# Performance work log

Hardware: AMD Instinct MI355X
Metric: run time of the kernel (lower is better)

## Reference

```python
import jax, jax.numpy as jnp
import numpy as np

GAMMA = 0.7
WALK_LEN = 3
TAU = 1.0
N_FILTERS = 8


def _row_norm(A):
    return A / jnp.clip(jnp.sum(A, axis=-1, keepdims=True), 1e-12, None)


def _motif_channel(A, idx, Wadj, gates):
    # A: [n,n]; idx: [I,k] int node indices; Wadj: [F,k,k]; gates: [L]
    n = A.shape[0]
    I, k = idx.shape
    F = Wadj.shape[0]
    # learnable filter adjacency: softplus, symmetrize, zero diagonal, row-normalize
    S = jax.nn.softplus(Wadj)
    S = 0.5 * (S + jnp.swapaxes(S, -1, -2)) * (1.0 - jnp.eye(k, dtype=A.dtype))
    Sf = _row_norm(S)                                  # [F,k,k]
    # per-instance induced subgraph transition matrices
    As = A[idx[:, :, None], idx[:, None, :]]           # [I,k,k]
    Tm = _row_norm(As)                                 # [I,k,k]
    # batched Kronecker product: Km[i,f,a*k+b,c*k+d] = Tm[i,a,c]*Sf[f,b,d]
    Km = (Tm[:, None, :, None, :, None] * Sf[None, :, None, :, None, :]).reshape(I, F, k * k, k * k)
    gp = jax.nn.softplus(gates)                        # [L] length gates
    M = Km
    acc = (GAMMA * gp[0]) * jnp.trace(M, axis1=-2, axis2=-1)   # [I,F]
    for p in range(2, WALK_LEN + 1):
        M = M @ Km
        acc = acc + (GAMMA ** p * gp[p - 1]) * jnp.trace(M, axis1=-2, axis2=-1)
    sims = acc                                         # [I,F] RWK similarities
    alphas = jax.nn.softmax(sims / max(1e-06, TAU), axis=-1)
    contrib = (alphas * sims) / float(k)               # [I,F]
    upd = jnp.broadcast_to(contrib[:, None, :], (I, k, F)).reshape(I * k, F)
    return jnp.zeros((n, F), A.dtype).at[idx.reshape(-1)].add(upd)


def _layer(A, tri_idx, cyc_idx, H, Wt, Wc, g, lng, lnb, w1, b1, w2, b2):
    Phi = jnp.concatenate([_motif_channel(A, tri_idx, Wt, g),
                           _motif_channel(A, cyc_idx, Wc, g),
                           H], axis=1)                 # [n, in_ch]
    mu = jnp.mean(Phi, axis=-1, keepdims=True)
    var = jnp.var(Phi, axis=-1, keepdims=True)
    X = (Phi - mu) / jnp.sqrt(var + 1e-5) * lng + lnb  # LayerNorm
    return jax.nn.gelu(X @ w1 + b1, approximate=False) @ w2 + b2  # dropout = identity (eval)


def _templates():
    tri = np.zeros((3, 3), np.float32)
    for u, v in [(0, 1), (1, 2), (0, 2)]:
        tri[u, v] = tri[v, u] = 1.0
    cyc = np.zeros((4, 4), np.float32)
    for u, v in [(0, 1), (1, 2), (2, 3), (3, 0)]:
        cyc[u, v] = cyc[v, u] = 1.0
    return tri, cyc


def setup_inputs() -> dict:
    key = jax.random.key(0)
    ks = jax.random.split(key, 16)
    n, D, HID = 4096, 128, 128
    A = (jax.random.uniform(ks[0], (n, n)) < 0.01).astype(jnp.float32)
    A = 0.5 * (A + A.T)
    A = A * (1.0 - jnp.eye(n, dtype=jnp.float32))
    tri_idx = jax.random.randint(ks[1], (30000, 3), 0, n, dtype=jnp.int32)
    cyc_idx = jax.random.randint(ks[2], (15000, 4), 0, n, dtype=jnp.int32)
    tri_t, cyc_t = _templates()
    def w_adj(k, tmpl):
        return jnp.asarray(tmpl)[None] + 0.05 * jax.random.normal(k, (N_FILTERS,) + tmpl.shape, dtype=jnp.float32)
    in0, in1 = 17, 145
    inp = {"A_full": A, "tri_idx": tri_idx, "cyc_idx": cyc_idx,
           "W_tri_0": w_adj(ks[3], tri_t), "W_cyc_0": w_adj(ks[4], cyc_t),
           "gates_0": jnp.zeros((WALK_LEN,), jnp.float32),
           "lng_0": jnp.ones((in0,), jnp.float32), "lnb_0": jnp.zeros((in0,), jnp.float32),
           "w1_0": 0.05 * jax.random.normal(ks[5], (in0, HID), jnp.float32), "b1_0": jnp.zeros((HID,), jnp.float32),
           "w2_0": 0.05 * jax.random.normal(ks[6], (HID, D), jnp.float32), "b2_0": jnp.zeros((D,), jnp.float32),
           "W_tri_1": w_adj(ks[7], tri_t), "W_cyc_1": w_adj(ks[8], cyc_t),
           "gates_1": jnp.zeros((WALK_LEN,), jnp.float32),
           "lng_1": jnp.ones((in1,), jnp.float32), "lnb_1": jnp.zeros((in1,), jnp.float32),
           "w1_1": 0.05 * jax.random.normal(ks[9], (in1, HID), jnp.float32), "b1_1": jnp.zeros((HID,), jnp.float32),
           "w2_1": 0.05 * jax.random.normal(ks[10], (HID, D), jnp.float32), "b2_1": jnp.zeros((D,), jnp.float32)}
    return inp


def reference(A_full, tri_idx, cyc_idx,
              W_tri_0, W_cyc_0, gates_0, lng_0, lnb_0, w1_0, b1_0, w2_0, b2_0,
              W_tri_1, W_cyc_1, gates_1, lng_1, lnb_1, w1_1, b1_1, w2_1, b2_1):
    # base channel (use_base=True): node degree from dense adjacency
    H = jnp.sum(A_full, axis=-1, keepdims=True)        # [n,1]
    Z = _layer(A_full, tri_idx, cyc_idx, H, W_tri_0, W_cyc_0, gates_0, lng_0, lnb_0, w1_0, b1_0, w2_0, b2_0)
    H = jnp.concatenate([Z, H], axis=1)                # residual_cat: [n,129]
    Z = _layer(A_full, tri_idx, cyc_idx, H, W_tri_1, W_cyc_1, gates_1, lng_1, lnb_1, w1_1, b1_1, w2_1, b2_1)
    H = jnp.concatenate([Z, H], axis=1)                # [n,257]
    return H
```

## Files before the change

### kernel.cpp

```cpp
#include <hip/hip_runtime.h>
#include <math.h>
#include <stdint.h>

#define GAMMA 0.7f
#define CAP 96

typedef __attribute__((ext_vector_type(8))) short short8v;
typedef __attribute__((ext_vector_type(4))) float f32x4;

__device__ __forceinline__ float sp_dev(float x) {
    return fmaxf(x, 0.0f) + log1pf(expf(-fabsf(x)));
}
__device__ __forceinline__ float gelu_exact(float x) {
    return 0.5f * x * (1.0f + erff(x * 0.70710678118654752f));
}
__device__ __forceinline__ uint16_t f2bf(float x) {
    union { float f; uint32_t u; } c; c.f = x;
    uint32_t u = c.u + 0x7FFFu + ((c.u >> 16) & 1u);
    return (uint16_t)(u >> 16);
}

__global__ void prep_kernel(const float* __restrict__ Wt0, const float* __restrict__ Wc0,
                            const float* __restrict__ g0,
                            const float* __restrict__ Wt1, const float* __restrict__ Wc1,
                            const float* __restrict__ g1,
                            const float* __restrict__ w1_0, const float* __restrict__ w2_0,
                            const float* __restrict__ w1_1, const float* __restrict__ w2_1,
                            float* __restrict__ dcoef,
                            uint16_t* __restrict__ Wb10, uint16_t* __restrict__ Wb20,
                            uint16_t* __restrict__ Wb11, uint16_t* __restrict__ Wb21,
                            int* __restrict__ cursor, int ncur) {
    int tid = threadIdx.x;
    int gtid = blockIdx.x * blockDim.x + tid;
    int stride = gridDim.x * blockDim.x;

    for (int i = gtid; i < ncur; i += stride) cursor[i] = 0;

    if (blockIdx.x == 0 && tid < 32) {
        int L = tid >> 4, m = (tid >> 3) & 1, f = tid & 7;
        int k = m ? 4 : 3;
        const float* W = L ? (m ? Wc1 : Wt1) : (m ? Wc0 : Wt0);
        const float* g = L ? g1 : g0;
        float S[4][4], Y[4][4];
        for (int a = 0; a < k; a++)
            for (int b = 0; b < k; b++)
                S[a][b] = sp_dev(W[(f * k + a) * k + b]);
        for (int a = 0; a < k; a++)
            for (int b = 0; b < k; b++)
                Y[a][b] = (a == b) ? 0.0f : 0.5f * (S[a][b] + S[b][a]);
        for (int a = 0; a < k; a++) {
            float rs = 0.0f;
            for (int b = 0; b < k; b++) rs += Y[a][b];
            rs = fmaxf(rs, 1e-12f);
            for (int b = 0; b < k; b++) Y[a][b] /= rs;
        }
        float t1 = 0, t2 = 0, t3 = 0;
        for (int a = 0; a < k; a++) t1 += Y[a][a];
        for (int a = 0; a < k; a++)
            for (int b = 0; b < k; b++) t2 += Y[a][b] * Y[b][a];
        for (int a = 0; a < k; a++)
            for (int b = 0; b < k; b++)
                for (int c = 0; c < k; c++) t3 += Y[a][b] * Y[b][c] * Y[c][a];
        float* d = dcoef + ((L * 2 + m) * 8 + f) * 3;
        d[0] = GAMMA * sp_dev(g[0]) * t1;
        d[1] = GAMMA * GAMMA * sp_dev(g[1]) * t2;
        d[2] = GAMMA * GAMMA * GAMMA * sp_dev(g[2]) * t3;
    }
    for (int idx = gtid; idx < 57344; idx += stride) {
        if (idx < 4096) {
            int c = idx >> 5, k = idx & 31;
            Wb10[idx] = (k < 17) ? f2bf(w1_0[k * 128 + c]) : 0;
        } else if (idx < 20480) {
            int e = idx - 4096; int c = e >> 7, k = e & 127;
            Wb20[e] = f2bf(w2_0[k * 128 + c]);
        } else if (idx < 40960) {
            int e = idx - 20480; int c = e / 160, k = e % 160;
            Wb11[e] = (k < 145) ? f2bf(w1_1[k * 128 + c]) : 0;
        } else {
            int e = idx - 40960; int c = e >> 7, k = e & 127;
            Wb21[e] = f2bf(w2_1[k * 128 + c]);
        }
    }
}

template <int K>
__device__ __forceinline__ void contrib_group(
    const float* __restrict__ A, int n,
    const int* __restrict__ idx, int I, int i, int g, int lane,
    const float (*dc)[8][3], float* __restrict__ cont,
    int* __restrict__ cursor, int* __restrict__ slotbuf) {
    int base = lane & ~3;
    int mynode = (g < K) ? idx[i * K + g] : 0;
    int nb0 = __shfl(mynode, base + 0);
    int nb1 = __shfl(mynode, base + 1);
    int nb2 = __shfl(mynode, base + 2);
    int nb3 = (K == 4) ? __shfl(mynode, base + 3) : 0;

    float r0, r1, r2, r3;
    if (K == 3) {
        if (g < 3) {
            const float* Ar = A + (size_t)mynode * n;
            r0 = Ar[nb0]; r1 = Ar[nb1]; r2 = Ar[nb2]; r3 = 0.0f;
        } else {
            r0 = 0.0f; r1 = 0.0f; r2 = 0.0f; r3 = 1.0f;
        }
    } else {
        const float* Ar = A + (size_t)mynode * n;
        r0 = Ar[nb0]; r1 = Ar[nb1]; r2 = Ar[nb2]; r3 = Ar[nb3];
    }
    float rs = fmaxf(r0 + r1 + r2 + r3, 1e-12f);
    float inv = 1.0f / rs;
    r0 *= inv; r1 *= inv; r2 *= inv; r3 *= inv;

    float M[4][4];
#pragma unroll
    for (int b = 0; b < 4; b++) {
        M[b][0] = __shfl(r0, base + b);
        M[b][1] = __shfl(r1, base + b);
        M[b][2] = __shfl(r2, base + b);
        M[b][3] = __shfl(r3, base + b);
    }

    float t1 = M[0][0] + M[1][1] + M[2][2] + M[3][3];
    float t2 = 0.0f, t3 = 0.0f;
#pragma unroll
    for (int a = 0; a < 4; a++)
#pragma unroll
        for (int b = 0; b < 4; b++) {
            float ab = M[a][b];
            t2 += ab * M[b][a];
#pragma unroll
            for (int c = 0; c < 4; c++) t3 += ab * M[b][c] * M[c][a];
        }
    if (K == 3) { t1 -= 1.0f; t2 -= 1.0f; t3 -= 1.0f; }

#pragma unroll
    for (int L = 0; L < 2; L++) {
        float sims[8], mx = -1e30f;
#pragma unroll
        for (int f = 0; f < 8; f++) {
            sims[f] = dc[L][f][0] * t1 + dc[L][f][1] * t2 + dc[L][f][2] * t3;
            mx = fmaxf(mx, sims[f]);
        }
        float es[8], se = 0.0f;
#pragma unroll
        for (int f = 0; f < 8; f++) { es[f] = expf(sims[f] - mx); se += es[f]; }
        float sinv = 1.0f / se;
        float cn[8];
#pragma unroll
        for (int f = 0; f < 8; f++) cn[f] = es[f] * sinv * sims[f] * (1.0f / (float)K);
        float p0 = (g == 0) ? cn[0] : (g == 1) ? cn[2] : (g == 2) ? cn[4] : cn[6];
        float p1 = (g == 0) ? cn[1] : (g == 1) ? cn[3] : (g == 2) ? cn[5] : cn[7];
        float2 st = make_float2(p0, p1);
        *(float2*)(cont + ((size_t)L * I + i) * 8 + 2 * g) = st;
    }

    if (g < K) {
        int pos = atomicAdd(&cursor[mynode], 1);
        if (pos < CAP) slotbuf[(size_t)mynode * CAP + pos] = i;
    }
}

__global__ __launch_bounds__(256) void fused_kernel(
    const float* __restrict__ A, int n,
    const int* __restrict__ tri, int Itri,
    const int* __restrict__ cyc, int Icyc,
    int Btri, int Bcyc,
    const float* __restrict__ dcoef,
    float* __restrict__ tri_c, float* __restrict__ cyc_c,
    int* __restrict__ cursor, int* __restrict__ slotbuf,
    float* __restrict__ H0, float* __restrict__ out) {
    __shared__ float dc[2][8][3];
    __shared__ float red[4];
    int bid = blockIdx.x;
    int tid = threadIdx.x;

    if (bid < Btri + Bcyc) {
        bool isTri = bid < Btri;
        const float* dl0 = dcoef + (isTri ? 0 : 24);
        const float* dl1 = dcoef + (isTri ? 48 : 72);
        if (tid < 24) dc[0][tid / 3][tid % 3] = dl0[tid];
        else if (tid < 48) { int t = tid - 24; dc[1][t / 3][t % 3] = dl1[t]; }
        __syncthreads();

        int lane = tid & 63;
        int g = tid & 3;
        if (isTri) {
            int i = bid * 64 + (tid >> 2);
            if (i < Itri)
                contrib_group<3>(A, n, tri, Itri, i, g, lane, dc, tri_c, cursor, slotbuf);
        } else {
            int i = (bid - Btri) * 64 + (tid >> 2);
            if (i < Icyc)
                contrib_group<4>(A, n, cyc, Icyc, i, g, lane, dc, cyc_c,
                                 cursor + n, slotbuf + (size_t)n * CAP);
        }
    } else {
        int row = bid - (Btri + Bcyc);
        const float4* Arow = (const float4*)(A + (size_t)row * n);
        int n4 = n >> 2;
        float s = 0.0f;
        for (int i = tid; i < n4; i += 256) {
            float4 v = Arow[i];
            s += v.x + v.y + v.z + v.w;
        }
        for (int off = 32; off > 0; off >>= 1) s += __shfl_down(s, off);
        if ((tid & 63) == 0) red[tid >> 6] = s;
        __syncthreads();
        if (tid == 0) {
            float t = red[0] + red[1] + red[2] + red[3];
            H0[row] = t;
            out[(size_t)row * 257 + 256] = t;
        }
    }
}

__global__ __launch_bounds__(512) void mega_kernel(
    const float* __restrict__ tri_c, int Itri,
    const float* __restrict__ cyc_c, int Icyc,
    const int* __restrict__ cursor, const int* __restrict__ slotbuf,
    const float* __restrict__ H0,
    const float* __restrict__ lng0, const float* __restrict__ lnb0,
    const uint16_t* __restrict__ Wb10, const float* __restrict__ b1_0,
    const uint16_t* __restrict__ Wb20, const float* __restrict__ b2_0,
    const float* __restrict__ lng1, const float* __restrict__ lnb1,
    const uint16_t* __restrict__ Wb11, const float* __restrict__ b1_1,
    const uint16_t* __restrict__ Wb21, const float* __restrict__ b2_1,
    float* __restrict__ out, int n) {
    __shared__ uint16_t Xs[16][168];
    __shared__ uint16_t Hs[16][136];
    __shared__ float    Zs[16][129];
    __shared__ float    phi0[16][17];
    __shared__ float    f1[16][16];
    __shared__ float    h0s[16];

    int tid = threadIdx.x;
    int v0 = blockIdx.x * 16;
    int wave = tid >> 6;
    int lane = tid & 63;
    int lr = lane & 15, lg = lane >> 4;

    {
        int r = tid >> 5;
        int combo = tid & 31;
        int m = combo >> 4, L = (combo >> 3) & 1, f = combo & 7;
        int v = v0 + r;
        int cnt = cursor[m * n + v];
        cnt = cnt < CAP ? cnt : CAP;
        const int* bucket = slotbuf + ((size_t)(m * n + v)) * CAP;
        const float* c = m ? cyc_c : tri_c;
        int I = m ? Icyc : Itri;
        float sum = 0.0f;
        for (int j = 0; j < cnt; j++) {
            int i = bucket[j];
            sum += c[((size_t)L * I + i) * 8 + f];
        }
        if (L == 0) phi0[r][m * 8 + f] = sum;
        else        f1[r][m * 8 + f] = sum;
        if (combo == 0) { float h = H0[v]; phi0[r][16] = h; h0s[r] = h; }
    }
    __syncthreads();

    {
        int r = tid >> 5;
        int j = tid & 31;
        float x = (j < 17) ? phi0[r][j] : 0.0f;
        float s1 = x, s2 = x * x;
        for (int o = 16; o > 0; o >>= 1) { s1 += __shfl_xor(s1, o); s2 += __shfl_xor(s2, o); }
        float mu = s1 / 17.0f;
        float rstd = rsqrtf(s2 / 17.0f - mu * mu + 1e-5f);
        Xs[r][j] = (j < 17) ? f2bf((x - mu) * rstd * lng0[j] + lnb0[j]) : (uint16_t)0;
    }
    __syncthreads();

    {
        int col = wave * 16 + lr;
        f32x4 acc = {0.f, 0.f, 0.f, 0.f};
        short8v a = *(const short8v*)&Xs[lr][lg * 8];
        short8v b = *(const short8v*)(Wb10 + (size_t)col * 32 + lg * 8);
        acc = __builtin_amdgcn_mfma_f32_16x16x32_bf16(a, b, acc, 0, 0, 0);
        float bias = b1_0[col];
#pragma unroll
        for (int i = 0; i < 4; i++)
            Hs[lg * 4 + i][col] = f2bf(gelu_exact(acc[i] + bias));
    }
    __syncthreads();

    {
        int col = wave * 16 + lr;
        f32x4 acc = {0.f, 0.f, 0.f, 0.f};
#pragma unroll
        for (int ks = 0; ks < 4; ks++) {
            short8v a = *(const short8v*)&Hs[lr][ks * 32 + lg * 8];
            short8v b = *(const short8v*)(Wb20 + (size_t)col * 128 + ks * 32 + lg * 8);
            acc = __builtin_amdgcn_mfma_f32_16x16x32_bf16(a, b, acc, 0, 0, 0);
        }
        float bias = b2_0[col];
#pragma unroll
        for (int i = 0; i < 4; i++) {
            int row = lg * 4 + i;
            float val = acc[i] + bias;
            out[(size_t)(v0 + row) * 257 + 128 + col] = val;
            Zs[row][col] = val;
        }
    }
    __syncthreads();

    {
        int rr = tid >> 5;
        int t = tid & 31;
        float ph[5];
        float s1 = 0.0f, s2 = 0.0f;
#pragma unroll
        for (int s = 0; s < 5; s++) {
            int j = t + 32 * s;
            float x = 0.0f;
            if (j < 16) x = f1[rr][j];
            else if (j < 144) x = Zs[rr][j - 16];
            else if (j == 144) x = h0s[rr];
            ph[s] = x;
            if (j < 145) { s1 += x; s2 += x * x; }
        }
        for (int o = 16; o > 0; o >>= 1) { s1 += __shfl_xor(s1, o); s2 += __shfl_xor(s2, o); }
        float mu = s1 / 145.0f;
        float rstd = rsqrtf(s2 / 145.0f - mu * mu + 1e-5f);
#pragma unroll
        for (int s = 0; s < 5; s++) {
            int j = t + 32 * s;
            Xs[rr][j] = (j < 145) ? f2bf((ph[s] - mu) * rstd * lng1[j] + lnb1[j]) : (uint16_t)0;
        }
    }
    __syncthreads();

    {
        int col = wave * 16 + lr;
        f32x4 acc = {0.f, 0.f, 0.f, 0.f};
#pragma unroll
        for (int ks = 0; ks < 5; ks++) {
            short8v a = *(const short8v*)&Xs[lr][ks * 32 + lg * 8];
            short8v b = *(const short8v*)(Wb11 + (size_t)col * 160 + ks * 32 + lg * 8);
            acc = __builtin_amdgcn_mfma_f32_16x16x32_bf16(a, b, acc, 0, 0, 0);
        }
        float bias = b1_1[col];
#pragma unroll
        for (int i = 0; i < 4; i++)
            Hs[lg * 4 + i][col] = f2bf(gelu_exact(acc[i] + bias));
    }
    __syncthreads();

    {
        int col = wave * 16 + lr;
        f32x4 acc = {0.f, 0.f, 0.f, 0.f};
#pragma unroll
        for (int ks = 0; ks < 4; ks++) {
            short8v a = *(const short8v*)&Hs[lr][ks * 32 + lg * 8];
            short8v b = *(const short8v*)(Wb21 + (size_t)col * 128 + ks * 32 + lg * 8);
            acc = __builtin_amdgcn_mfma_f32_16x16x32_bf16(a, b, acc, 0, 0, 0);
        }
        float bias = b2_1[col];
#pragma unroll
        for (int i = 0; i < 4; i++) {
            int row = lg * 4 + i;
            out[(size_t)(v0 + row) * 257 + col] = acc[i] + bias;
        }
    }
}

extern "C" void kernel_launch(void* const* d_in, const int* in_sizes, int n_in,
                              void* d_out, int out_size, void* d_ws, size_t ws_size,
                              hipStream_t stream) {
    const float* A    = (const float*)d_in[0];
    const int*   tri  = (const int*)d_in[1];
    const int*   cyc  = (const int*)d_in[2];
    const float* Wt0  = (const float*)d_in[3];
    const float* Wc0  = (const float*)d_in[4];
    const float* g0   = (const float*)d_in[5];
    const float* lng0 = (const float*)d_in[6];
    const float* lnb0 = (const float*)d_in[7];
    const float* w1_0 = (const float*)d_in[8];
    const float* b1_0 = (const float*)d_in[9];
    const float* w2_0 = (const float*)d_in[10];
    const float* b2_0 = (const float*)d_in[11];
    const float* Wt1  = (const float*)d_in[12];
    const float* Wc1  = (const float*)d_in[13];
    const float* g1   = (const float*)d_in[14];
    const float* lng1 = (const float*)d_in[15];
    const float* lnb1 = (const float*)d_in[16];
    const float* w1_1 = (const float*)d_in[17];
    const float* b1_1 = (const float*)d_in[18];
    const float* w2_1 = (const float*)d_in[19];
    const float* b2_1 = (const float*)d_in[20];

    int n    = out_size / 257;
    int Itri = in_sizes[1] / 3;
    int Icyc = in_sizes[2] / 4;

    float* ws    = (float*)d_ws;
    float* dcoef = ws;
    float* H0    = ws + 128;
    float* tri_c = H0 + n;
    float* cyc_c = tri_c + (size_t)2 * Itri * 8;
    int*   cursor  = (int*)(cyc_c + (size_t)2 * Icyc * 8);
    int*   slotbuf = cursor + (size_t)2 * n;
    uint16_t* Wb10 = (uint16_t*)(slotbuf + (size_t)2 * n * CAP);
    uint16_t* Wb20 = Wb10 + 128 * 32;
    uint16_t* Wb11 = Wb20 + 128 * 128;
    uint16_t* Wb21 = Wb11 + 128 * 160;
    float* out = (float*)d_out;

    prep_kernel<<<64, 256, 0, stream>>>(Wt0, Wc0, g0, Wt1, Wc1, g1,
                                        w1_0, w2_0, w1_1, w2_1,
                                        dcoef, Wb10, Wb20, Wb11, Wb21,
                                        cursor, 2 * n);

    int Btri = (Itri + 63) / 64;
    int Bcyc = (Icyc + 63) / 64;
    fused_kernel<<<Btri + Bcyc + n, 256, 0, stream>>>(
        A, n, tri, Itri, cyc, Icyc, Btri, Bcyc, dcoef,
        tri_c, cyc_c, cursor, slotbuf, H0, out);

    mega_kernel<<<n / 16, 512, 0, stream>>>(
        tri_c, Itri, cyc_c, Icyc, cursor, slotbuf, H0,
        lng0, lnb0, Wb10, b1_0, Wb20, b2_0,
        lng1, lnb1, Wb11, b1_1, Wb21, b2_1, out, n);
}
```

Measured before the change: 72.86 us.

## Merge three kernels into one cooperative persistent kernel with grid syncs

Replaces the prep, fused and mega kernels with one cooperative kernel of 256 blocks of 512 threads that uses grid.sync between phases. Each block recomputes the filter coefficients into shared memory rather than exchanging them through global memory. Motif instances and degree rows are split across the persistent blocks, and the MLP node tiles are looped over. The aim is to remove launch overhead and inter-kernel gaps, at the cost of grid-barrier latency, a fixed grid size, and lower parallelism in phases that previously used many more blocks.

```diff
diff --git a/kernel.cpp b/kernel.cpp
--- a/kernel.cpp
+++ b/kernel.cpp
@@ -1,9 +1,14 @@
 #include <hip/hip_runtime.h>
+#include <hip/hip_cooperative_groups.h>
 #include <math.h>
 #include <stdint.h>
 
+namespace cg = cooperative_groups;
+
 #define GAMMA 0.7f
 #define CAP 96
+#define NBLK 256
+#define NTHR 512
 
 typedef __attribute__((ext_vector_type(8))) short short8v;
 typedef __attribute__((ext_vector_type(4))) float f32x4;
@@ -20,27 +25,118 @@
     return (uint16_t)(u >> 16);
 }
 
-__global__ void prep_kernel(const float* __restrict__ Wt0, const float* __restrict__ Wc0,
-                            const float* __restrict__ g0,
-                            const float* __restrict__ Wt1, const float* __restrict__ Wc1,
-                            const float* __restrict__ g1,
-                            const float* __restrict__ w1_0, const float* __restrict__ w2_0,
-                            const float* __restrict__ w1_1, const float* __restrict__ w2_1,
-                            float* __restrict__ dcoef,
-                            uint16_t* __restrict__ Wb10, uint16_t* __restrict__ Wb20,
-                            uint16_t* __restrict__ Wb11, uint16_t* __restrict__ Wb21,
-                            int* __restrict__ cursor, int ncur) {
-    int tid = threadIdx.x;
-    int gtid = blockIdx.x * blockDim.x + tid;
-    int stride = gridDim.x * blockDim.x;
-
-    for (int i = gtid; i < ncur; i += stride) cursor[i] = 0;
-
-    if (blockIdx.x == 0 && tid < 32) {
+template <int K>
+__device__ __forceinline__ void contrib_group(
+    const float* __restrict__ A, int n,
+    const int* __restrict__ idx, int I, int i, int g, int lane,
+    const float (*dc)[8][3], float* __restrict__ cont,
+    int* __restrict__ cursor, int* __restrict__ slotbuf) {
+    int base = lane & ~3;
+    int mynode = (g < K) ? idx[i * K + g] : 0;
+    int nb0 = __shfl(mynode, base + 0);
+    int nb1 = __shfl(mynode, base + 1);
+    int nb2 = __shfl(mynode, base + 2);
+    int nb3 = (K == 4) ? __shfl(mynode, base + 3) : 0;
+
+    float r0, r1, r2, r3;
+    if (K == 3) {
+        if (g < 3) {
+            const float* Ar = A + (size_t)mynode * n;
+            r0 = Ar[nb0]; r1 = Ar[nb1]; r2 = Ar[nb2]; r3 = 0.0f;
+        } else {
+            r0 = 0.0f; r1 = 0.0f; r2 = 0.0f; r3 = 1.0f;
+        }
+    } else {
+        const float* Ar = A + (size_t)mynode * n;
+        r0 = Ar[nb0]; r1 = Ar[nb1]; r2 = Ar[nb2]; r3 = Ar[nb3];
+    }
+    float rs = fmaxf(r0 + r1 + r2 + r3, 1e-12f);
+    float inv = 1.0f / rs;
+    r0 *= inv; r1 *= inv; r2 *= inv; r3 *= inv;
+
+    float M[4][4];
+#pragma unroll
+    for (int b = 0; b < 4; b++) {
+        M[b][0] = __shfl(r0, base + b);
+        M[b][1] = __shfl(r1, base + b);
+        M[b][2] = __shfl(r2, base + b);
+        M[b][3] = __shfl(r3, base + b);
+    }
+
+    float t1 = M[0][0] + M[1][1] + M[2][2] + M[3][3];
+    float t2 = 0.0f, t3 = 0.0f;
+#pragma unroll
+    for (int a = 0; a < 4; a++)
+#pragma unroll
+        for (int b = 0; b < 4; b++) {
+            float ab = M[a][b];
+            t2 += ab * M[b][a];
+#pragma unroll
+            for (int c = 0; c < 4; c++) t3 += ab * M[b][c] * M[c][a];
+        }
+    if (K == 3) { t1 -= 1.0f; t2 -= 1.0f; t3 -= 1.0f; }
+
+#pragma unroll
+    for (int L = 0; L < 2; L++) {
+        float sims[8], mx = -1e30f;
+#pragma unroll
+        for (int f = 0; f < 8; f++) {
+            sims[f] = dc[L][f][0] * t1 + dc[L][f][1] * t2 + dc[L][f][2] * t3;
+            mx = fmaxf(mx, sims[f]);
+        }
+        float es[8], se = 0.0f;
+#pragma unroll
+        for (int f = 0; f < 8; f++) { es[f] = expf(sims[f] - mx); se += es[f]; }
+        float sinv = 1.0f / se;
+        float cn[8];
+#pragma unroll
+        for (int f = 0; f < 8; f++) cn[f] = es[f] * sinv * sims[f] * (1.0f / (float)K);
+        float p0 = (g == 0) ? cn[0] : (g == 1) ? cn[2] : (g == 2) ? cn[4] : cn[6];
+        float p1 = (g == 0) ? cn[1] : (g == 1) ? cn[3] : (g == 2) ? cn[5] : cn[7];
+        *(float2*)(cont + ((size_t)L * I + i) * 8 + 2 * g) = make_float2(p0, p1);
+    }
+
+    if (g < K) {
+        int pos = atomicAdd(&cursor[mynode], 1);
+        if (pos < CAP) slotbuf[(size_t)mynode * CAP + pos] = i;
+    }
+}
+
+struct KParams {
+    const float* A; const int* tri; const int* cyc;
+    const float *Wt0, *Wc0, *g0, *lng0, *lnb0, *w1_0, *b1_0, *w2_0, *b2_0;
+    const float *Wt1, *Wc1, *g1, *lng1, *lnb1, *w1_1, *b1_1, *w2_1, *b2_1;
+    float* H0; float* tri_c; float* cyc_c;
+    int* cursor; int* slotbuf;
+    uint16_t *Wb10, *Wb20, *Wb11, *Wb21;
+    float* out;
+    int n, Itri, Icyc;
+};
+
+__global__ __launch_bounds__(NTHR, 2) void uber_kernel(KParams p) {
+    cg::grid_group grid = cg::this_grid();
+    __shared__ float    dcs[2][2][8][3];
+    __shared__ uint16_t Xs[16][168];
+    __shared__ uint16_t Hs[16][136];
+    __shared__ float    Zs[16][129];
+    __shared__ float    phi0[16][17];
+    __shared__ float    f1[16][16];
+    __shared__ float    h0s[16];
+
+    const int tid = threadIdx.x;
+    const int bid = blockIdx.x;
+    const int nb = gridDim.x;
+    const int gtid = bid * NTHR + tid;
+    const int gstride = nb * NTHR;
+    const int n = p.n;
+
+    for (int i = gtid; i < 2 * n; i += gstride) p.cursor[i] = 0;
+
+    if (tid < 32) {
         int L = tid >> 4, m = (tid >> 3) & 1, f = tid & 7;
         int k = m ? 4 : 3;
-        const float* W = L ? (m ? Wc1 : Wt1) : (m ? Wc0 : Wt0);
-        const float* g = L ? g1 : g0;
+        const float* W = L ? (m ? p.Wc1 : p.Wt1) : (m ? p.Wc0 : p.Wt0);
+        const float* g = L ? p.g1 : p.g0;
         float S[4][4], Y[4][4];
         for (int a = 0; a < k; a++)
             for (int b = 0; b < k; b++)
@@ -61,366 +157,243 @@
         for (int a = 0; a < k; a++)
             for (int b = 0; b < k; b++)
                 for (int c = 0; c < k; c++) t3 += Y[a][b] * Y[b][c] * Y[c][a];
-        float* d = dcoef + ((L * 2 + m) * 8 + f) * 3;
-        d[0] = GAMMA * sp_dev(g[0]) * t1;
-        d[1] = GAMMA * GAMMA * sp_dev(g[1]) * t2;
-        d[2] = GAMMA * GAMMA * GAMMA * sp_dev(g[2]) * t3;
-    }
-    for (int idx = gtid; idx < 57344; idx += stride) {
+        dcs[m][L][f][0] = GAMMA * sp_dev(g[0]) * t1;
+        dcs[m][L][f][1] = GAMMA * GAMMA * sp_dev(g[1]) * t2;
+        dcs[m][L][f][2] = GAMMA * GAMMA * GAMMA * sp_dev(g[2]) * t3;
+    }
+
+    for (int idx = gtid; idx < 57344; idx += gstride) {
         if (idx < 4096) {
             int c = idx >> 5, k = idx & 31;
-            Wb10[idx] = (k < 17) ? f2bf(w1_0[k * 128 + c]) : 0;
+            p.Wb10[idx] = (k < 17) ? f2bf(p.w1_0[k * 128 + c]) : 0;
         } else if (idx < 20480) {
             int e = idx - 4096; int c = e >> 7, k = e & 127;
-            Wb20[e] = f2bf(w2_0[k * 128 + c]);
+            p.Wb20[e] = f2bf(p.w2_0[k * 128 + c]);
         } else if (idx < 40960) {
             int e = idx - 20480; int c = e / 160, k = e % 160;
-            Wb11[e] = (k < 145) ? f2bf(w1_1[k * 128 + c]) : 0;
+            p.Wb11[e] = (k < 145) ? f2bf(p.w1_1[k * 128 + c]) : 0;
         } else {
             int e = idx - 40960; int c = e >> 7, k = e & 127;
-            Wb21[e] = f2bf(w2_1[k * 128 + c]);
-        }
-    }
-}
-
-template <int K>
-__device__ __forceinline__ void contrib_group(
-    const float* __restrict__ A, int n,
-    const int* __restrict__ idx, int I, int i, int g, int lane,
-    const float (*dc)[8][3], float* __restrict__ cont,
-    int* __restrict__ cursor, int* __restrict__ slotbuf) {
-    int base = lane & ~3;
-    int mynode = (g < K) ? idx[i * K + g] : 0;
-    int nb0 = __shfl(mynode, base + 0);
-    int nb1 = __shfl(mynode, base + 1);
-    int nb2 = __shfl(mynode, base + 2);
-    int nb3 = (K == 4) ? __shfl(mynode, base + 3) : 0;
-
-    float r0, r1, r2, r3;
-    if (K == 3) {
-        if (g < 3) {
-            const float* Ar = A + (size_t)mynode * n;
-            r0 = Ar[nb0]; r1 = Ar[nb1]; r2 = Ar[nb2]; r3 = 0.0f;
-        } else {
-            r0 = 0.0f; r1 = 0.0f; r2 = 0.0f; r3 = 1.0f;
-        }
-    } else {
-        const float* Ar = A + (size_t)mynode * n;
-        r0 = Ar[nb0]; r1 = Ar[nb1]; r2 = Ar[nb2]; r3 = Ar[nb3];
-    }
-    float rs = fmaxf(r0 + r1 + r2 + r3, 1e-12f);
-    float inv = 1.0f / rs;
-    r0 *= inv; r1 *= inv; r2 *= inv; r3 *= inv;
-
-    float M[4][4];
-#pragma unroll
-    for (int b = 0; b < 4; b++) {
-        M[b][0] = __shfl(r0, base + b);
-        M[b][1] = __shfl(r1, base + b);
-        M[b][2] = __shfl(r2, base + b);
-        M[b][3] = __shfl(r3, base + b);
-    }
-
-    float t1 = M[0][0] + M[1][1] + M[2][2] + M[3][3];
-    float t2 = 0.0f, t3 = 0.0f;
-#pragma unroll
-    for (int a = 0; a < 4; a++)
-#pragma unroll
-        for (int b = 0; b < 4; b++) {
-            float ab = M[a][b];
-            t2 += ab * M[b][a];
-#pragma unroll
-            for (int c = 0; c < 4; c++) t3 += ab * M[b][c] * M[c][a];
-        }
-    if (K == 3) { t1 -= 1.0f; t2 -= 1.0f; t3 -= 1.0f; }
-
-#pragma unroll
-    for (int L = 0; L < 2; L++) {
-        float sims[8], mx = -1e30f;
-#pragma unroll
-        for (int f = 0; f < 8; f++) {
-            sims[f] = dc[L][f][0] * t1 + dc[L][f][1] * t2 + dc[L][f][2] * t3;
-            mx = fmaxf(mx, sims[f]);
-        }
-        float es[8], se = 0.0f;
-#pragma unroll
-        for (int f = 0; f < 8; f++) { es[f] = expf(sims[f] - mx); se += es[f]; }
-        float sinv = 1.0f / se;
-        float cn[8];
-#pragma unroll
-        for (int f = 0; f < 8; f++) cn[f] = es[f] * sinv * sims[f] * (1.0f / (float)K);
-        float p0 = (g == 0) ? cn[0] : (g == 1) ? cn[2] : (g == 2) ? cn[4] : cn[6];
-        float p1 = (g == 0) ? cn[1] : (g == 1) ? cn[3] : (g == 2) ? cn[5] : cn[7];
-        float2 st = make_float2(p0, p1);
-        *(float2*)(cont + ((size_t)L * I + i) * 8 + 2 * g) = st;
-    }
-
-    if (g < K) {
-        int pos = atomicAdd(&cursor[mynode], 1);
-        if (pos < CAP) slotbuf[(size_t)mynode * CAP + pos] = i;
-    }
-}
-
-__global__ __launch_bounds__(256) void fused_kernel(
-    const float* __restrict__ A, int n,
-    const int* __restrict__ tri, int Itri,
-    const int* __restrict__ cyc, int Icyc,
-    int Btri, int Bcyc,
-    const float* __restrict__ dcoef,
-    float* __restrict__ tri_c, float* __restrict__ cyc_c,
-    int* __restrict__ cursor, int* __restrict__ slotbuf,
-    float* __restrict__ H0, float* __restrict__ out) {
-    __shared__ float dc[2][8][3];
-    __shared__ float red[4];
-    int bid = blockIdx.x;
-    int tid = threadIdx.x;
-
-    if (bid < Btri + Bcyc) {
-        bool isTri = bid < Btri;
-        const float* dl0 = dcoef + (isTri ? 0 : 24);
-        const float* dl1 = dcoef + (isTri ? 48 : 72);
-        if (tid < 24) dc[0][tid / 3][tid % 3] = dl0[tid];
-        else if (tid < 48) { int t = tid - 24; dc[1][t / 3][t % 3] = dl1[t]; }
-        __syncthreads();
-
+            p.Wb21[e] = f2bf(p.w2_1[k * 128 + c]);
+        }
+    }
+
+    grid.sync();
+
+    {
+        int lane = tid & 63, g = tid & 3;
+        int per = (p.Itri + nb - 1) / nb;
+        int lim = bid * per + per;
+        if (lim > p.Itri) lim = p.Itri;
+        for (int q = bid * per + (tid >> 2); q < lim; q += NTHR / 4)
+            contrib_group<3>(p.A, n, p.tri, p.Itri, q, g, lane, dcs[0],
+                             p.tri_c, p.cursor, p.slotbuf);
+        per = (p.Icyc + nb - 1) / nb;
+        lim = bid * per + per;
+        if (lim > p.Icyc) lim = p.Icyc;
+        for (int q = bid * per + (tid >> 2); q < lim; q += NTHR / 4)
+            contrib_group<4>(p.A, n, p.cyc, p.Icyc, q, g, lane, dcs[1],
+                             p.cyc_c, p.cursor + n, p.slotbuf + (size_t)n * CAP);
+    }
+    {
+        int wave = tid >> 6, lane = tid & 63;
+        int n4 = n >> 2;
+        for (int row = bid * 8 + wave; row < n; row += nb * 8) {
+            const float4* Ar = (const float4*)(p.A + (size_t)row * n);
+            float s = 0.0f;
+            for (int i = lane; i < n4; i += 64) {
+                float4 v = Ar[i];
+                s += v.x + v.y + v.z + v.w;
+            }
+            for (int off = 32; off > 0; off >>= 1) s += __shfl_down(s, off);
+            if (lane == 0) {
+                p.H0[row] = s;
+                p.out[(size_t)row * 257 + 256] = s;
+            }
+        }
+    }
+
+    grid.sync();
+
+    const int ntiles = n / 16;
+    for (int t = bid; t < ntiles; t += nb) {
+        int v0 = t * 16;
+        int wave = tid >> 6;
         int lane = tid & 63;
-        int g = tid & 3;
-        if (isTri) {
-            int i = bid * 64 + (tid >> 2);
-            if (i < Itri)
-                contrib_group<3>(A, n, tri, Itri, i, g, lane, dc, tri_c, cursor, slotbuf);
-        } else {
-            int i = (bid - Btri) * 64 + (tid >> 2);
-            if (i < Icyc)
-                contrib_group<4>(A, n, cyc, Icyc, i, g, lane, dc, cyc_c,
-                                 cursor + n, slotbuf + (size_t)n * CAP);
-        }
-    } else {
-        int row = bid - (Btri + Bcyc);
-        const float4* Arow = (const float4*)(A + (size_t)row * n);
-        int n4 = n >> 2;
-        float s = 0.0f;
-        for (int i = tid; i < n4; i += 256) {
-            float4 v = Arow[i];
-            s += v.x + v.y + v.z + v.w;
-        }
-        for (int off = 32; off > 0; off >>= 1) s += __shfl_down(s, off);
-        if ((tid & 63) == 0) red[tid >> 6] = s;
-        __syncthreads();
-        if (tid == 0) {
-            float t = red[0] + red[1] + red[2] + red[3];
-            H0[row] = t;
-            out[(size_t)row * 257 + 256] = t;
-        }
-    }
-}
-
-__global__ __launch_bounds__(512) void mega_kernel(
-    const float* __restrict__ tri_c, int Itri,
-    const float* __restrict__ cyc_c, int Icyc,
-    const int* __restrict__ cursor, const int* __restrict__ slotbuf,
-    const float* __restrict__ H0,
-    const float* __restrict__ lng0, const float* __restrict__ lnb0,
-    const uint16_t* __restrict__ Wb10, const float* __restrict__ b1_0,
-    const uint16_t* __restrict__ Wb20, const float* __restrict__ b2_0,
-    const float* __restrict__ lng1, const float* __restrict__ lnb1,
-    const uint16_t* __restrict__ Wb11, const float* __restrict__ b1_1,
-    const uint16_t* __restrict__ Wb21, const float* __restrict__ b2_1,
-    float* __restrict__ out, int n) {
-    __shared__ uint16_t Xs[16][168];
-    __shared__ uint16_t Hs[16][136];
-    __shared__ float    Zs[16][129];
-    __shared__ float    phi0[16][17];
-    __shared__ float    f1[16][16];
-    __shared__ float    h0s[16];
-
-    int tid = threadIdx.x;
-    int v0 = blockIdx.x * 16;
-    int wave = tid >> 6;
-    int lane = tid & 63;
-    int lr = lane & 15, lg = lane >> 4;
-
-    {
-        int r = tid >> 5;
-        int combo = tid & 31;
-        int m = combo >> 4, L = (combo >> 3) & 1, f = combo & 7;
-        int v = v0 + r;
-        int cnt = cursor[m * n + v];
-        cnt = cnt < CAP ? cnt : CAP;
-        const int* bucket = slotbuf + ((size_t)(m * n + v)) * CAP;
-        const float* c = m ? cyc_c : tri_c;
-        int I = m ? Icyc : Itri;
-        float sum = 0.0f;
-        for (int j = 0; j < cnt; j++) {
-            int i = bucket[j];
-            sum += c[((size_t)L * I + i) * 8 + f];
-        }
-        if (L == 0) phi0[r][m * 8 + f] = sum;
-        else        f1[r][m * 8 + f] = sum;
-        if (combo == 0) { float h = H0[v]; phi0[r][16] = h; h0s[r] = h; }
-    }
-    __syncthreads();
-
-    {
-        int r = tid >> 5;
-        int j = tid & 31;
-        float x = (j < 17) ? phi0[r][j] : 0.0f;
-        float s1 = x, s2 = x * x;
-        for (int o = 16; o > 0; o >>= 1) { s1 += __shfl_xor(s1, o); s2 += __shfl_xor(s2, o); }
-        float mu = s1 / 17.0f;
-        float rstd = rsqrtf(s2 / 17.0f - mu * mu + 1e-5f);
-        Xs[r][j] = (j < 17) ? f2bf((x - mu) * rstd * lng0[j] + lnb0[j]) : (uint16_t)0;
-    }
-    __syncthreads();
-
-    {
-        int col = wave * 16 + lr;
-        f32x4 acc = {0.f, 0.f, 0.f, 0.f};
-        short8v a = *(const short8v*)&Xs[lr][lg * 8];
-        short8v b = *(const short8v*)(Wb10 + (size_t)col * 32 + lg * 8);
-        acc = __builtin_amdgcn_mfma_f32_16x16x32_bf16(a, b, acc, 0, 0, 0);
-        float bias = b1_0[col];
-#pragma unroll
-        for (int i = 0; i < 4; i++)
-            Hs[lg * 4 + i][col] = f2bf(gelu_exact(acc[i] + bias));
-    }
-    __syncthreads();
-
-    {
-        int col = wave * 16 + lr;
-        f32x4 acc = {0.f, 0.f, 0.f, 0.f};
-#pragma unroll
-        for (int ks = 0; ks < 4; ks++) {
-            short8v a = *(const short8v*)&Hs[lr][ks * 32 + lg * 8];
-            short8v b = *(const short8v*)(Wb20 + (size_t)col * 128 + ks * 32 + lg * 8);
+        int lr = lane & 15, lg = lane >> 4;
+
+        {
+            int r = tid >> 5;
+            int combo = tid & 31;
+            int m = combo >> 4, L = (combo >> 3) & 1, f = combo & 7;
+            int v = v0 + r;
+            int cnt = p.cursor[m * n + v];
+            cnt = cnt < CAP ? cnt : CAP;
+            const int* bucket = p.slotbuf + ((size_t)(m * n + v)) * CAP;
+            const float* c = m ? p.cyc_c : p.tri_c;
+            int I = m ? p.Icyc : p.Itri;
+            float sum = 0.0f;
+            for (int j = 0; j < cnt; j++) {
+                int i = bucket[j];
+                sum += c[((size_t)L * I + i) * 8 + f];
+            }
+            if (L == 0) phi0[r][m * 8 + f] = sum;
+            else        f1[r][m * 8 + f] = sum;
+            if (combo == 0) { float h = p.H0[v]; phi0[r][16] = h; h0s[r] = h; }
+        }
+        __syncthreads();
+
+        {
+            int r = tid >> 5;
+            int j = tid & 31;
+            float x = (j < 17) ? phi0[r][j] : 0.0f;
+            float s1 = x, s2 = x * x;
+            for (int o = 16; o > 0; o >>= 1) { s1 += __shfl_xor(s1, o); s2 += __shfl_xor(s2, o); }
+            float mu = s1 / 17.0f;
+            float rstd = rsqrtf(s2 / 17.0f - mu * mu + 1e-5f);
+            Xs[r][j] = (j < 17) ? f2bf((x - mu) * rstd * p.lng0[j] + p.lnb0[j]) : (uint16_t)0;
+        }
+        __syncthreads();
+
+        {
+            int col = wave * 16 + lr;
+            f32x4 acc = {0.f, 0.f, 0.f, 0.f};
+            short8v a = *(const short8v*)&Xs[lr][lg * 8];
+            short8v b = *(const short8v*)(p.Wb10 + (size_t)col * 32 + lg * 8);
             acc = __builtin_amdgcn_mfma_f32_16x16x32_bf16(a, b, acc, 0, 0, 0);
-        }
-        float bias = b2_0[col];
-#pragma unroll
-        for (int i = 0; i < 4; i++) {
-            int row = lg * 4 + i;
-            float val = acc[i] + bias;
-            out[(size_t)(v0 + row) * 257 + 128 + col] = val;
-            Zs[row][col] = val;
-        }
-    }
-    __syncthreads();
-
-    {
-        int rr = tid >> 5;
-        int t = tid & 31;
-        float ph[5];
-        float s1 = 0.0f, s2 = 0.0f;
-#pragma unroll
-        for (int s = 0; s < 5; s++) {
-            int j = t + 32 * s;
-            float x = 0.0f;
-            if (j < 16) x = f1[rr][j];
-            else if (j < 144) x = Zs[rr][j - 16];
-            else if (j == 144) x = h0s[rr];
-            ph[s] = x;
-            if (j < 145) { s1 += x; s2 += x * x; }
-        }
-        for (int o = 16; o > 0; o >>= 1) { s1 += __shfl_xor(s1, o); s2 += __shfl_xor(s2, o); }
-        float mu = s1 / 145.0f;
-        float rstd = rsqrtf(s2 / 145.0f - mu * mu + 1e-5f);
-#pragma unroll
-        for (int s = 0; s < 5; s++) {
-            int j = t + 32 * s;
-            Xs[rr][j] = (j < 145) ? f2bf((ph[s] - mu) * rstd * lng1[j] + lnb1[j]) : (uint16_t)0;
-        }
-    }
-    __syncthreads();
-
-    {
-        int col = wave * 16 + lr;
-        f32x4 acc = {0.f, 0.f, 0.f, 0.f};
-#pragma unroll
-        for (int ks = 0; ks < 5; ks++) {
-            short8v a = *(const short8v*)&Xs[lr][ks * 32 + lg * 8];
-            short8v b = *(const short8v*)(Wb11 + (size_t)col * 160 + ks * 32 + lg * 8);
-            acc = __builtin_amdgcn_mfma_f32_16x16x32_bf16(a, b, acc, 0, 0, 0);
-        }
-        float bias = b1_1[col];
-#pragma unroll
-        for (int i = 0; i < 4; i++)
-            Hs[lg * 4 + i][col] = f2bf(gelu_exact(acc[i] + bias));
-    }
-    __syncthreads();
-
-    {
-        int col = wave * 16 + lr;
-        f32x4 acc = {0.f, 0.f, 0.f, 0.f};
-#pragma unroll
-        for (int ks = 0; ks < 4; ks++) {
-            short8v a = *(const short8v*)&Hs[lr][ks * 32 + lg * 8];
-            short8v b = *(const short8v*)(Wb21 + (size_t)col * 128 + ks * 32 + lg * 8);
-            acc = __builtin_amdgcn_mfma_f32_16x16x32_bf16(a, b, acc, 0, 0, 0);
-        }
-        float bias = b2_1[col];
-#pragma unroll
-        for (int i = 0; i < 4; i++) {
-            int row = lg * 4 + i;
-            out[(size_t)(v0 + row) * 257 + col] = acc[i] + bias;
-        }
+            float bias = p.b1_0[col];
+#pragma unroll
+            for (int i = 0; i < 4; i++)
+                Hs[lg * 4 + i][col] = f2bf(gelu_exact(acc[i] + bias));
+        }
+        __syncthreads();
+
+        {
+            int col = wave * 16 + lr;
+            f32x4 acc = {0.f, 0.f, 0.f, 0.f};
+#pragma unroll
+            for (int ks = 0; ks < 4; ks++) {
+                short8v a = *(const short8v*)&Hs[lr][ks * 32 + lg * 8];
+                short8v b = *(const short8v*)(p.Wb20 + (size_t)col * 128 + ks * 32 + lg * 8);
+                acc = __builtin_amdgcn_mfma_f32_16x16x32_bf16(a, b, acc, 0, 0, 0);
+            }
+            float bias = p.b2_0[col];
+#pragma unroll
+            for (int i = 0; i < 4; i++) {
+                int row = lg * 4 + i;
+                float val = acc[i] + bias;
+                p.out[(size_t)(v0 + row) * 257 + 128 + col] = val;
+                Zs[row][col] = val;
+            }
+        }
+        __syncthreads();
+
+        {
+            int rr = tid >> 5;
+            int tt = tid & 31;
+            float ph[5];
+            float s1 = 0.0f, s2 = 0.0f;
+#pragma unroll
+            for (int s = 0; s < 5; s++) {
+                int j = tt + 32 * s;
+                float x = 0.0f;
+                if (j < 16) x = f1[rr][j];
+                else if (j < 144) x = Zs[rr][j - 16];
+                else if (j == 144) x = h0s[rr];
+                ph[s] = x;
+                if (j < 145) { s1 += x; s2 += x * x; }
+            }
+            for (int o = 16; o > 0; o >>= 1) { s1 += __shfl_xor(s1, o); s2 += __shfl_xor(s2, o); }
+            float mu = s1 / 145.0f;
+            float rstd = rsqrtf(s2 / 145.0f - mu * mu + 1e-5f);
+#pragma unroll
+            for (int s = 0; s < 5; s++) {
+                int j = tt + 32 * s;
+                Xs[rr][j] = (j < 145) ? f2bf((ph[s] - mu) * rstd * p.lng1[j] + p.lnb1[j]) : (uint16_t)0;
+            }
+        }
+        __syncthreads();
+
+        {
+            int col = wave * 16 + lr;
+            f32x4 acc = {0.f, 0.f, 0.f, 0.f};
+#pragma unroll
+            for (int ks = 0; ks < 5; ks++) {
+                short8v a = *(const short8v*)&Xs[lr][ks * 32 + lg * 8];
+                short8v b = *(const short8v*)(p.Wb11 + (size_t)col * 160 + ks * 32 + lg * 8);
+                acc = __builtin_amdgcn_mfma_f32_16x16x32_bf16(a, b, acc, 0, 0, 0);
+            }
+            float bias = p.b1_1[col];
+#pragma unroll
+            for (int i = 0; i < 4; i++)
+                Hs[lg * 4 + i][col] = f2bf(gelu_exact(acc[i] + bias));
+        }
+        __syncthreads();
+
+        {
+            int col = wave * 16 + lr;
+            f32x4 acc = {0.f, 0.f, 0.f, 0.f};
+#pragma unroll
+            for (int ks = 0; ks < 4; ks++) {
+                short8v a = *(const short8v*)&Hs[lr][ks * 32 + lg * 8];
+                short8v b = *(const short8v*)(p.Wb21 + (size_t)col * 128 + ks * 32 + lg * 8);
+                acc = __builtin_amdgcn_mfma_f32_16x16x32_bf16(a, b, acc, 0, 0, 0);
+            }
+            float bias = p.b2_1[col];
+#pragma unroll
+            for (int i = 0; i < 4; i++) {
+                int row = lg * 4 + i;
+                p.out[(size_t)(v0 + row) * 257 + col] = acc[i] + bias;
+            }
+        }
+        __syncthreads();
     }
 }
 
 extern "C" void kernel_launch(void* const* d_in, const int* in_sizes, int n_in,
                               void* d_out, int out_size, void* d_ws, size_t ws_size,
                               hipStream_t stream) {
-    const float* A    = (const float*)d_in[0];
-    const int*   tri  = (const int*)d_in[1];
-    const int*   cyc  = (const int*)d_in[2];
-    const float* Wt0  = (const float*)d_in[3];
-    const float* Wc0  = (const float*)d_in[4];
-    const float* g0   = (const float*)d_in[5];
-    const float* lng0 = (const float*)d_in[6];
-    const float* lnb0 = (const float*)d_in[7];
-    const float* w1_0 = (const float*)d_in[8];
-    const float* b1_0 = (const float*)d_in[9];
-    const float* w2_0 = (const float*)d_in[10];
-    const float* b2_0 = (const float*)d_in[11];
-    const float* Wt1  = (const float*)d_in[12];
-    const float* Wc1  = (const float*)d_in[13];
-    const float* g1   = (const float*)d_in[14];
-    const float* lng1 = (const float*)d_in[15];
-    const float* lnb1 = (const float*)d_in[16];
-    const float* w1_1 = (const float*)d_in[17];
-    const float* b1_1 = (const float*)d_in[18];
-    const float* w2_1 = (const float*)d_in[19];
-    const float* b2_1 = (const float*)d_in[20];
-
     int n    = out_size / 257;
     int Itri = in_sizes[1] / 3;
     int Icyc = in_sizes[2] / 4;
 
-    float* ws    = (float*)d_ws;
-    float* dcoef = ws;
-    float* H0    = ws + 128;
-    float* tri_c = H0 + n;
-    float* cyc_c = tri_c + (size_t)2 * Itri * 8;
-    int*   cursor  = (int*)(cyc_c + (size_t)2 * Icyc * 8);
-    int*   slotbuf = cursor + (size_t)2 * n;
-    uint16_t* Wb10 = (uint16_t*)(slotbuf + (size_t)2 * n * CAP);
-    uint16_t* Wb20 = Wb10 + 128 * 32;
-    uint16_t* Wb11 = Wb20 + 128 * 128;
-    uint16_t* Wb21 = Wb11 + 128 * 160;
-    float* out = (float*)d_out;
-
-    prep_kernel<<<64, 256, 0, stream>>>(Wt0, Wc0, g0, Wt1, Wc1, g1,
-                                        w1_0, w2_0, w1_1, w2_1,
-                                        dcoef, Wb10, Wb20, Wb11, Wb21,
-                                        cursor, 2 * n);
-
-    int Btri = (Itri + 63) / 64;
-    int Bcyc = (Icyc + 63) / 64;
-    fused_kernel<<<Btri + Bcyc + n, 256, 0, stream>>>(
-        A, n, tri, Itri, cyc, Icyc, Btri, Bcyc, dcoef,
-        tri_c, cyc_c, cursor, slotbuf, H0, out);
-
-    mega_kernel<<<n / 16, 512, 0, stream>>>(
-        tri_c, Itri, cyc_c, Icyc, cursor, slotbuf, H0,
-        lng0, lnb0, Wb10, b1_0, Wb20, b2_0,
-        lng1, lnb1, Wb11, b1_1, Wb21, b2_1, out, n);
-}
+    float* ws = (float*)d_ws;
+    KParams hp;
+    hp.A    = (const float*)d_in[0];
+    hp.tri  = (const int*)d_in[1];
+    hp.cyc  = (const int*)d_in[2];
+    hp.Wt0  = (const float*)d_in[3];
+    hp.Wc0  = (const float*)d_in[4];
+    hp.g0   = (const float*)d_in[5];
+    hp.lng0 = (const float*)d_in[6];
+    hp.lnb0 = (const float*)d_in[7];
+    hp.w1_0 = (const float*)d_in[8];
+    hp.b1_0 = (const float*)d_in[9];
+    hp.w2_0 = (const float*)d_in[10];
+    hp.b2_0 = (const float*)d_in[11];
+    hp.Wt1  = (const float*)d_in[12];
+    hp.Wc1  = (const float*)d_in[13];
+    hp.g1   = (const float*)d_in[14];
+    hp.lng1 = (const float*)d_in[15];
+    hp.lnb1 = (const float*)d_in[16];
+    hp.w1_1 = (const float*)d_in[17];
+    hp.b1_1 = (const float*)d_in[18];
+    hp.w2_1 = (const float*)d_in[19];
+    hp.b2_1 = (const float*)d_in[20];
+
+    hp.H0    = ws;
+    hp.tri_c = ws + n;
+    hp.cyc_c = hp.tri_c + (size_t)2 * Itri * 8;
+    hp.cursor  = (int*)(hp.cyc_c + (size_t)2 * Icyc * 8);
+    hp.slotbuf = hp.cursor + (size_t)2 * n;
+    hp.Wb10 = (uint16_t*)(hp.slotbuf + (size_t)2 * n * CAP);
+    hp.Wb20 = hp.Wb10 + 128 * 32;
+    hp.Wb11 = hp.Wb20 + 128 * 128;
+    hp.Wb21 = hp.Wb11 + 128 * 160;
+    hp.out  = (float*)d_out;
+    hp.n = n; hp.Itri = Itri; hp.Icyc = Icyc;
+
+    void* kargs[] = { (void*)&hp };
+    hipLaunchCooperativeKernel((const void*)uber_kernel, dim3(NBLK), dim3(NTHR),
+                               kargs, 0, stream);
+}
```

New measurement: 145.1 us. +99.2%, slower.
